# Optimization experiments

Hardware: AMD Instinct MI355X
Metric: run time of the kernel (lower is better)

Reference implementation:

```python
import jax, jax.numpy as jnp
import numpy as np


def setup_inputs() -> dict:
    key = jax.random.key(0)
    k1, k2, k3, k4 = jax.random.split(key, 4)
    B, S, D = 32, 512, 768
    return {
        "image": jax.random.normal(k1, (B, S, D), dtype=jnp.float32),
        "text": jax.random.normal(k2, (B, S, D), dtype=jnp.float32),
        "target": jax.random.normal(k3, (B, S, D), dtype=jnp.float32),
        "padding_mask": jax.random.randint(k4, (B, S), 0, 2, dtype=jnp.int32),
    }


def reference(image, text, target, padding_mask):
    D = image.shape[-1]
    # Drop BOS / CLS position for the text<->target alignment.
    txt = text[:, 1:]                      # [B, S-1, D]
    tgt = target[:, 1:]                    # [B, S-1, D]
    pm = padding_mask[:, 1:]               # [B, S-1]

    # Cosine similarity: normalize then batched matmul.
    txt_n = txt / jnp.linalg.norm(txt, axis=-1, keepdims=True)
    tgt_n = tgt / jnp.linalg.norm(tgt, axis=-1, keepdims=True)
    sim = jnp.einsum('bid,bjd->bij', txt_n, tgt_n)   # [B, S-1, S-1]

    # For each text token, pick the best-matching target patch.
    idx = jnp.argmax(sim, axis=-1)                   # [B, S-1]
    aligned = jnp.take_along_axis(tgt, idx[..., None], axis=1)  # [B, S-1, D]

    # Masked MSE over non-padded tokens (mask==1 means padded in torch code).
    valid = (pm == 0).astype(jnp.float32)            # [B, S-1]
    diff2 = jnp.square(txt.astype(jnp.float32) - aligned.astype(jnp.float32))
    kd_text_loss = jnp.sum(diff2 * valid[..., None]) / (jnp.sum(valid) * D)

    # Plain MSE between image tokens and full target.
    kd_image_loss = jnp.mean(jnp.square(image.astype(jnp.float32) - target.astype(jnp.float32)))

    total_loss = (kd_text_loss + kd_image_loss) / 2
    return total_loss, kd_text_loss, kd_image_loss, idx
```

## Files before the change

kernel.cpp:

```cpp
#include <hip/hip_runtime.h>
#include <math.h>

#define B       32
#define S_FULL  512
#define S       511
#define D       768
#define NROWS   (B * S)

#define TM 128
#define TN 128
#define NCHUNK 4
#define NKT 24
#define EPS_MARGIN 6e-5f
#define SIM_SCALE  512.0f
#define SIM_SCALE2 (SIM_SCALE * SIM_SCALE)

#define NPREP   (B * S_FULL / 4)
#define NRBLK   512

typedef __attribute__((ext_vector_type(8))) _Float16 f16x8;
typedef __attribute__((ext_vector_type(4))) float f32x4;

__device__ inline void cvt8(const float4& v0, const float4& v1, float s,
                            f16x8& hv, f16x8& lv) {
    float x[8] = {v0.x, v0.y, v0.z, v0.w, v1.x, v1.y, v1.z, v1.w};
    #pragma unroll
    for (int e = 0; e < 8; ++e) {
        float xs = x[e] * s;
        _Float16 h = (_Float16)xs;
        hv[e] = h;
        lv[e] = (_Float16)(xs - (float)h);
    }
}

__global__ __launch_bounds__(256) void prep_kernel(
    const float* __restrict__ image, const float* __restrict__ text,
    const float* __restrict__ target,
    float* __restrict__ inv_t, float* __restrict__ inv_g, float* __restrict__ pimg,
    float* __restrict__ ctrl)
{
    __shared__ float warr[4];
    if (blockIdx.x == 0) ctrl[threadIdx.x] = 0.f;
    int w    = threadIdx.x >> 6;
    int row  = blockIdx.x * 4 + w;
    int lane = threadIdx.x & 63;
    int b = row >> 9, i = row & 511;
    const float4* pi4 = (const float4*)(image  + (size_t)row * D);
    const float4* pt4 = (const float4*)(text   + (size_t)row * D);
    const float4* pg4 = (const float4*)(target + (size_t)row * D);
    float st = 0.f, sg = 0.f, si = 0.f;
    #pragma unroll
    for (int q = 0; q < 3; ++q) {
        float4 a = pt4[lane + 64 * q];
        float4 g = pg4[lane + 64 * q];
        float4 m = pi4[lane + 64 * q];
        st += a.x*a.x + a.y*a.y + a.z*a.z + a.w*a.w;
        sg += g.x*g.x + g.y*g.y + g.z*g.z + g.w*g.w;
        float dx = m.x-g.x, dy = m.y-g.y, dz = m.z-g.z, dw = m.w-g.w;
        si += dx*dx + dy*dy + dz*dz + dw*dw;
    }
    #pragma unroll
    for (int m = 32; m > 0; m >>= 1) {
        st += __shfl_xor(st, m); sg += __shfl_xor(sg, m); si += __shfl_xor(si, m);
    }
    if (lane == 0) {
        warr[w] = si;
        if (i >= 1) {
            int r = b * S + i - 1;
            inv_t[r] = (st > 0.f) ? 1.f / sqrtf(st) : 0.f;
            inv_g[r] = (sg > 0.f) ? 1.f / sqrtf(sg) : 0.f;
        }
    }
    __syncthreads();
    if (threadIdx.x == 0)
        pimg[blockIdx.x] = warr[0] + warr[1] + warr[2] + warr[3];
}

__global__ __launch_bounds__(256, 2) void simargmax_kernel(
    const float* __restrict__ text, const float* __restrict__ target,
    const float* __restrict__ inv_t, const float* __restrict__ inv_g,
    float* __restrict__ pv, float* __restrict__ ps, int* __restrict__ pj)
{
    __shared__ __align__(16) _Float16 As[TM * 64];
    __shared__ __align__(16) _Float16 Bs[TM * 64];

    const int i0 = blockIdx.x * TM;
    const int jc = blockIdx.y;
    const int j0 = jc * TN;
    const int b  = blockIdx.z;
    const int t  = threadIdx.x;
    const int lane = t & 63;
    const int wy = t >> 6;
    const int quad = lane >> 4, cid = lane & 15;

    const float* Abase = text   + (size_t)b * S_FULL * D + D;
    const float* Bbase = target + (size_t)b * S_FULL * D + D;

    const int r0 = t >> 2;
    const int c0 = t & 3;
    const int kq = c0 * 8;

    float sa[2], sb[2];
    #pragma unroll
    for (int h = 0; h < 2; ++h) {
        int gi = i0 + r0 + 64 * h;
        sa[h] = (gi < S) ? inv_t[b * S + gi] * SIM_SCALE : 0.f;
        int gj = j0 + r0 + 64 * h;
        sb[h] = (gj < S) ? inv_g[b * S + gj] * SIM_SCALE : 0.f;
    }

    const int sw8 = (r0 & 7) * 8;
    const int fw8 = (cid & 7) * 8;
    const int qh  = quad * 8;

    f32x4 acc[2][8];
    #pragma unroll
    for (int mt = 0; mt < 2; ++mt)
        #pragma unroll
        for (int nt = 0; nt < 8; ++nt)
            acc[mt][nt] = (f32x4){0.f, 0.f, 0.f, 0.f};

    for (int kt = 0; kt < NKT; ++kt) {
        const int k0 = kt * 32;
        float4 va[2][2], vb[2][2];
        #pragma unroll
        for (int h = 0; h < 2; ++h) {
            int gi = i0 + r0 + 64 * h;
            if (gi < S) {
                const float4* pa = (const float4*)(Abase + (size_t)gi * D + k0 + kq);
                va[h][0] = pa[0]; va[h][1] = pa[1];
            } else {
                va[h][0] = make_float4(0.f,0.f,0.f,0.f);
                va[h][1] = make_float4(0.f,0.f,0.f,0.f);
            }
            int gj = j0 + r0 + 64 * h;
            if (gj < S) {
                const float4* pb = (const float4*)(Bbase + (size_t)gj * D + k0 + kq);
                vb[h][0] = pb[0]; vb[h][1] = pb[1];
            } else {
                vb[h][0] = make_float4(0.f,0.f,0.f,0.f);
                vb[h][1] = make_float4(0.f,0.f,0.f,0.f);
            }
        }
        __syncthreads();
        #pragma unroll
        for (int h = 0; h < 2; ++h) {
            int base = (r0 + 64 * h) * 64;
            f16x8 hv, lv;
            cvt8(va[h][0], va[h][1], sa[h], hv, lv);
            *(f16x8*)&As[base + ((c0 * 8)      ^ sw8)] = hv;
            *(f16x8*)&As[base + ((32 + c0 * 8) ^ sw8)] = lv;
            cvt8(vb[h][0], vb[h][1], sb[h], hv, lv);
            *(f16x8*)&Bs[base + ((c0 * 8)      ^ sw8)] = hv;
            *(f16x8*)&Bs[base + ((32 + c0 * 8) ^ sw8)] = lv;
        }
        __syncthreads();

        f16x8 ah[2], al[2];
        #pragma unroll
        for (int mt = 0; mt < 2; ++mt) {
            int ad = (wy * 32 + mt * 16 + cid) * 64;
            ah[mt] = *(const f16x8*)&As[ad + ( qh       ^ fw8)];
            al[mt] = *(const f16x8*)&As[ad + ((32 + qh) ^ fw8)];
        }
        #pragma unroll
        for (int nt = 0; nt < 8; ++nt) {
            int bd = (nt * 16 + cid) * 64;
            f16x8 bh = *(const f16x8*)&Bs[bd + ( qh       ^ fw8)];
            f16x8 bl = *(const f16x8*)&Bs[bd + ((32 + qh) ^ fw8)];
            #pragma unroll
            for (int mt = 0; mt < 2; ++mt) {
                acc[mt][nt] = __builtin_amdgcn_mfma_f32_16x16x32_f16(ah[mt], bh, acc[mt][nt], 0, 0, 0);
                acc[mt][nt] = __builtin_amdgcn_mfma_f32_16x16x32_f16(ah[mt], bl, acc[mt][nt], 0, 0, 0);
                acc[mt][nt] = __builtin_amdgcn_mfma_f32_16x16x32_f16(al[mt], bh, acc[mt][nt], 0, 0, 0);
            }
        }
    }

    #pragma unroll
    for (int mt = 0; mt < 2; ++mt) {
        #pragma unroll
        for (int r = 0; r < 4; ++r) {
            float v1 = -INFINITY, v2 = -INFINITY; int j1 = -1;
            #pragma unroll
            for (int nt = 0; nt < 8; ++nt) {
                int col = j0 + nt * 16 + cid;
                float v = acc[mt][nt][r];
                if (col < S) {
                    if (v > v1) { v2 = v1; v1 = v; j1 = col; }
                    else if (v > v2) v2 = v;
                }
            }
            #pragma unroll
            for (int m = 1; m < 16; m <<= 1) {
                float ov1 = __shfl_xor(v1, m);
                int   oj1 = __shfl_xor(j1, m);
                float ov2 = __shfl_xor(v2, m);
                if (ov1 > v1) { v2 = fmaxf(v1, ov2); v1 = ov1; j1 = oj1; }
                else          { v2 = fmaxf(v2, ov1); }
            }
            if (cid == 0) {
                int gi = i0 + wy * 32 + mt * 16 + quad * 4 + r;
                if (gi < S) {
                    size_t o = ((size_t)(b * S + gi) << 2) + jc;
                    pv[o] = v1; ps[o] = v2; pj[o] = j1;
                }
            }
        }
    }
}

__global__ __launch_bounds__(256) void text_kernel(
    const float* __restrict__ text, const float* __restrict__ target,
    const int* __restrict__ pm,
    const float* __restrict__ pv, const float* __restrict__ ps, const int* __restrict__ pj,
    float* __restrict__ idx_f, float* __restrict__ acc,
    int* __restrict__ list, int* __restrict__ cnt)
{
    __shared__ float ls[4], lc[4];
    int w   = threadIdx.x >> 6;
    int row = blockIdx.x * 4 + w;
    int lane = threadIdx.x & 63;
    int b = row / S, i = row - b * S;

    float v1 = -INFINITY, v2 = -INFINITY; int j1 = 0;
    #pragma unroll
    for (int c = 0; c < NCHUNK; ++c) {
        size_t o = ((size_t)row << 2) + c;
        float a1 = pv[o], a2 = ps[o]; int aj = pj[o];
        if (a1 > v1) { v2 = fmaxf(v1, a2); v1 = a1; j1 = aj; }
        else         { v2 = fmaxf(v2, a1); }
    }

    float s = 0.f, c1 = 0.f;
    if (v1 - v2 < EPS_MARGIN * SIM_SCALE2) {
        if (lane == 0) { int p = atomicAdd(cnt, 1); list[p] = row; }
    } else {
        if (lane == 0) idx_f[row] = (float)j1;
        if (pm[b * S_FULL + i + 1] == 0) {
            const float4* pt = (const float4*)(text   + (size_t)(b * S_FULL + i  + 1) * D);
            const float4* pg = (const float4*)(target + (size_t)(b * S_FULL + j1 + 1) * D);
            #pragma unroll
            for (int q = 0; q < 3; ++q) {
                float4 a = pt[lane + 64 * q];
                float4 g = pg[lane + 64 * q];
                float dx = a.x-g.x, dy = a.y-g.y, dz = a.z-g.z, dw = a.w-g.w;
                s += dx*dx + dy*dy + dz*dz + dw*dw;
            }
            #pragma unroll
            for (int m = 32; m > 0; m >>= 1) s += __shfl_xor(s, m);
            c1 = 1.f;
        }
    }
    if (lane == 0) { ls[w] = s; lc[w] = c1; }
    __syncthreads();
    if (threadIdx.x == 0) {
        float S4 = ls[0] + ls[1] + ls[2] + ls[3];
        float C4 = lc[0] + lc[1] + lc[2] + lc[3];
        if (C4 > 0.f) {
            atomicAdd(&acc[64  + (blockIdx.x & 63)], S4);
            atomicAdd(&acc[128 + (blockIdx.x & 63)], C4);
        }
    }
}

__global__ __launch_bounds__(256) void recheck_kernel(
    const float* __restrict__ text, const float* __restrict__ target,
    const int* __restrict__ pm, const float* __restrict__ inv_g,
    const int* __restrict__ list, const int* __restrict__ cnt,
    float* __restrict__ idx_f, float* __restrict__ acc,
    int* __restrict__ done, const float* __restrict__ pimg,
    float* __restrict__ out)
{
    __shared__ float wv[4];
    __shared__ int   wj[4];
    __shared__ int   bjf;
    __shared__ int   islast;
    const int t = threadIdx.x, w = t >> 6, lane = t & 63;
    const int n = *cnt;
    for (int it = blockIdx.x; it < n; it += gridDim.x) {
        int row = list[it];
        int b = row / S, i = row - b * S;
        const float4* tp = (const float4*)(text + (size_t)(b * S_FULL + i + 1) * D);
        float4 tr0 = tp[lane], tr1 = tp[lane + 64], tr2 = tp[lane + 128];
        const float* Gb = target + (size_t)b * S_FULL * D + D;
        const float* ig = inv_g + b * S;

        float bv = -INFINITY; int bj = 0;
        for (int j = w; j < S; j += 8) {
            const float4* g0 = (const float4*)(Gb + (size_t)j * D);
            int j2 = j + 4; bool ok2 = (j2 < S);
            const float4* g1 = (const float4*)(Gb + (size_t)(ok2 ? j2 : j) * D);
            float4 a0 = g0[lane], a1 = g0[lane + 64], a2 = g0[lane + 128];
            float4 c0 = g1[lane], c1 = g1[lane + 64], c2 = g1[lane + 128];
            float s0 = tr0.x*a0.x + tr0.y*a0.y + tr0.z*a0.z + tr0.w*a0.w
                     + tr1.x*a1.x + tr1.y*a1.y + tr1.z*a1.z + tr1.w*a1.w
                     + tr2.x*a2.x + tr2.y*a2.y + tr2.z*a2.z + tr2.w*a2.w;
            float s1 = tr0.x*c0.x + tr0.y*c0.y + tr0.z*c0.z + tr0.w*c0.w
                     + tr1.x*c1.x + tr1.y*c1.y + tr1.z*c1.z + tr1.w*c1.w
                     + tr2.x*c2.x + tr2.y*c2.y + tr2.z*c2.z + tr2.w*c2.w;
            #pragma unroll
            for (int m = 32; m > 0; m >>= 1) {
                s0 += __shfl_xor(s0, m);
                s1 += __shfl_xor(s1, m);
            }
            s0 *= ig[j];
            if (s0 > bv) { bv = s0; bj = j; }
            if (ok2) {
                s1 *= ig[j2];
                if (s1 > bv) { bv = s1; bj = j2; }
            }
        }
        if (lane == 0) { wv[w] = bv; wj[w] = bj; }
        __syncthreads();
        if (t == 0) {
            float fv = wv[0]; int fj = wj[0];
            #pragma unroll
            for (int q = 1; q < 4; ++q)
                if (wv[q] > fv || (wv[q] == fv && wj[q] < fj)) { fv = wv[q]; fj = wj[q]; }
            bjf = fj;
            idx_f[row] = (float)fj;
        }
        __syncthreads();
        if (w == 0 && pm[b * S_FULL + i + 1] == 0) {
            const float4* gp = (const float4*)(Gb + (size_t)bjf * D);
            float4 a0 = gp[lane], a1 = gp[lane + 64], a2 = gp[lane + 128];
            float dx, s = 0.f;
            dx = tr0.x-a0.x; s += dx*dx;  dx = tr0.y-a0.y; s += dx*dx;
            dx = tr0.z-a0.z; s += dx*dx;  dx = tr0.w-a0.w; s += dx*dx;
            dx = tr1.x-a1.x; s += dx*dx;  dx = tr1.y-a1.y; s += dx*dx;
            dx = tr1.z-a1.z; s += dx*dx;  dx = tr1.w-a1.w; s += dx*dx;
            dx = tr2.x-a2.x; s += dx*dx;  dx = tr2.y-a2.y; s += dx*dx;
            dx = tr2.z-a2.z; s += dx*dx;  dx = tr2.w-a2.w; s += dx*dx;
            #pragma unroll
            for (int m = 32; m > 0; m >>= 1) s += __shfl_xor(s, m);
            if (lane == 0) {
                atomicAdd(&acc[64  + (blockIdx.x & 63)], s);
                atomicAdd(&acc[128 + (blockIdx.x & 63)], 1.0f);
            }
        }
        __syncthreads();
    }

    if (t == 0) {
        __threadfence();
        int prev = atomicAdd(done, 1);
        islast = (prev == (int)gridDim.x - 1);
    }
    __syncthreads();
    if (!islast) return;
    __threadfence();
    {
        __shared__ float r[12];
        float si = 0.f;
        for (int i = t; i < NPREP; i += 256) si += pimg[i];
        float st = (t < 64) ? atomicAdd(&acc[64 + t],  0.0f) : 0.f;
        float sc = (t < 64) ? atomicAdd(&acc[128 + t], 0.0f) : 0.f;
        #pragma unroll
        for (int m = 32; m > 0; m >>= 1) {
            si += __shfl_xor(si, m);
            st += __shfl_xor(st, m);
            sc += __shfl_xor(sc, m);
        }
        if (lane == 0) { r[w] = si; r[4 + w] = st; r[8 + w] = sc; }
        __syncthreads();
        if (t == 0) {
            si = r[0] + r[1] + r[2] + r[3];
            st = r[4] + r[5] + r[6] + r[7];
            sc = r[8] + r[9] + r[10] + r[11];
            float img = si / (float)((size_t)B * S_FULL * D);
            float txt = st / (sc * (float)D);
            out[0] = 0.5f * (txt + img);
            out[1] = txt;
            out[2] = img;
        }
    }
}

extern "C" void kernel_launch(void* const* d_in, const int* in_sizes, int n_in,
                              void* d_out, int out_size, void* d_ws, size_t ws_size,
                              hipStream_t stream) {
    const float* image  = (const float*)d_in[0];
    const float* text   = (const float*)d_in[1];
    const float* target = (const float*)d_in[2];
    const int*   pm     = (const int*)d_in[3];
    float* out = (float*)d_out;

    float* ws    = (float*)d_ws;
    float* inv_t = ws;
    float* inv_g = ws + NROWS;
    float* pv    = ws + 2 * NROWS;
    float* ps    = ws + 6 * NROWS;
    int*   pj    = (int*)(ws + 10 * NROWS);
    int*   list  = (int*)(ws + 14 * NROWS);
    float* ctrl  = ws + 15 * NROWS;
    int*   cnt   = (int*)ctrl;
    int*   done  = (int*)ctrl + 1;
    float* acc   = ctrl + 64;
    float* pimg  = ctrl + 256;

    prep_kernel<<<NPREP, 256, 0, stream>>>(image, text, target, inv_t, inv_g, pimg, ctrl);
    simargmax_kernel<<<dim3(4, NCHUNK, B), 256, 0, stream>>>(
        text, target, inv_t, inv_g, pv, ps, pj);
    text_kernel<<<(NROWS + 3) / 4, 256, 0, stream>>>(
        text, target, pm, pv, ps, pj, out + 3, acc, list, cnt);
    recheck_kernel<<<NRBLK, 256, 0, stream>>>(
        text, target, pm, inv_g, list, cnt, out + 3, acc, done, pimg, out);
}
```

Measured before the change: 310.2 us.

## Assign one target row per lane in recheck, staging text row in LDS

The recheck kernel now stages the text row in shared memory and gives each lane its own target row, so each lane computes a full 768-wide dot product serially. Previously each wave split one dot product across lanes and reduced it with shuffles. This removes the per-candidate shuffle reductions and keeps them only for the final argmax. In exchange, each lane now reads a separate row of target with strided, uncoalesced loads, and the order of floating-point summation changes.

Result: no change. 305.3 us (-1.6%).

```diff
diff --git a/kernel.cpp b/kernel.cpp
--- a/kernel.cpp
+++ b/kernel.cpp
@@ -272,6 +272,7 @@
     int* __restrict__ done, const float* __restrict__ pimg,
     float* __restrict__ out)
 {
+    __shared__ __align__(16) float txt_lds[D];
     __shared__ float wv[4];
     __shared__ int   wj[4];
     __shared__ int   bjf;
@@ -281,35 +282,39 @@
     for (int it = blockIdx.x; it < n; it += gridDim.x) {
         int row = list[it];
         int b = row / S, i = row - b * S;
-        const float4* tp = (const float4*)(text + (size_t)(b * S_FULL + i + 1) * D);
-        float4 tr0 = tp[lane], tr1 = tp[lane + 64], tr2 = tp[lane + 128];
+        const float4* tp4 = (const float4*)(text + (size_t)(b * S_FULL + i + 1) * D);
+        if (t < D / 4) ((float4*)txt_lds)[t] = tp4[t];
+        __syncthreads();
         const float* Gb = target + (size_t)b * S_FULL * D + D;
         const float* ig = inv_g + b * S;
+        const float4* tl = (const float4*)txt_lds;
 
         float bv = -INFINITY; int bj = 0;
-        for (int j = w; j < S; j += 8) {
-            const float4* g0 = (const float4*)(Gb + (size_t)j * D);
-            int j2 = j + 4; bool ok2 = (j2 < S);
-            const float4* g1 = (const float4*)(Gb + (size_t)(ok2 ? j2 : j) * D);
-            float4 a0 = g0[lane], a1 = g0[lane + 64], a2 = g0[lane + 128];
-            float4 c0 = g1[lane], c1 = g1[lane + 64], c2 = g1[lane + 128];
-            float s0 = tr0.x*a0.x + tr0.y*a0.y + tr0.z*a0.z + tr0.w*a0.w
-                     + tr1.x*a1.x + tr1.y*a1.y + tr1.z*a1.z + tr1.w*a1.w
-                     + tr2.x*a2.x + tr2.y*a2.y + tr2.z*a2.z + tr2.w*a2.w;
-            float s1 = tr0.x*c0.x + tr0.y*c0.y + tr0.z*c0.z + tr0.w*c0.w
-                     + tr1.x*c1.x + tr1.y*c1.y + tr1.z*c1.z + tr1.w*c1.w
-                     + tr2.x*c2.x + tr2.y*c2.y + tr2.z*c2.z + tr2.w*c2.w;
-            #pragma unroll
-            for (int m = 32; m > 0; m >>= 1) {
-                s0 += __shfl_xor(s0, m);
-                s1 += __shfl_xor(s1, m);
-            }
-            s0 *= ig[j];
-            if (s0 > bv) { bv = s0; bj = j; }
-            if (ok2) {
-                s1 *= ig[j2];
-                if (s1 > bv) { bv = s1; bj = j2; }
-            }
+        #pragma unroll
+        for (int p = 0; p < 2; ++p) {
+            int j = w * 128 + p * 64 + lane;
+            if (j < S) {
+                const float4* gp = (const float4*)(Gb + (size_t)j * D);
+                float a0 = 0.f, a1 = 0.f, a2 = 0.f, a3 = 0.f;
+                for (int d = 0; d < D / 4; d += 4) {
+                    float4 g0 = gp[d],     t0 = tl[d];
+                    float4 g1 = gp[d + 1], t1 = tl[d + 1];
+                    float4 g2 = gp[d + 2], t2 = tl[d + 2];
+                    float4 g3 = gp[d + 3], t3 = tl[d + 3];
+                    a0 += g0.x*t0.x + g0.y*t0.y + g0.z*t0.z + g0.w*t0.w;
+                    a1 += g1.x*t1.x + g1.y*t1.y + g1.z*t1.z + g1.w*t1.w;
+                    a2 += g2.x*t2.x + g2.y*t2.y + g2.z*t2.z + g2.w*t2.w;
+                    a3 += g3.x*t3.x + g3.y*t3.y + g3.z*t3.z + g3.w*t3.w;
+                }
+                float s = ((a0 + a1) + (a2 + a3)) * ig[j];
+                if (s > bv || (s == bv && j < bj)) { bv = s; bj = j; }
+            }
+        }
+        #pragma unroll
+        for (int m = 32; m > 0; m >>= 1) {
+            float ov = __shfl_xor(bv, m);
+            int   oj = __shfl_xor(bj, m);
+            if (ov > bv || (ov == bv && oj < bj)) { bv = ov; bj = oj; }
         }
         if (lane == 0) { wv[w] = bv; wj[w] = bj; }
         __syncthreads();
@@ -323,15 +328,15 @@
         }
         __syncthreads();
         if (w == 0 && pm[b * S_FULL + i + 1] == 0) {
-            const float4* gp = (const float4*)(Gb + (size_t)bjf * D);
-            float4 a0 = gp[lane], a1 = gp[lane + 64], a2 = gp[lane + 128];
-            float dx, s = 0.f;
-            dx = tr0.x-a0.x; s += dx*dx;  dx = tr0.y-a0.y; s += dx*dx;
-            dx = tr0.z-a0.z; s += dx*dx;  dx = tr0.w-a0.w; s += dx*dx;
-            dx = tr1.x-a1.x; s += dx*dx;  dx = tr1.y-a1.y; s += dx*dx;
-            dx = tr1.z-a1.z; s += dx*dx;  dx = tr1.w-a1.w; s += dx*dx;
-            dx = tr2.x-a2.x; s += dx*dx;  dx = tr2.y-a2.y; s += dx*dx;
-            dx = tr2.z-a2.z; s += dx*dx;  dx = tr2.w-a2.w; s += dx*dx;
+            const float4* gp2 = (const float4*)(Gb + (size_t)bjf * D);
+            float s = 0.f;
+            #pragma unroll
+            for (int q = 0; q < 3; ++q) {
+                float4 a = tl[lane + 64 * q];
+                float4 g = gp2[lane + 64 * q];
+                float dx = a.x-g.x, dy = a.y-g.y, dz = a.z-g.z, dw = a.w-g.w;
+                s += dx*dx + dy*dy + dz*dz + dw*dw;
+            }
             #pragma unroll
             for (int m = 32; m > 0; m >>= 1) s += __shfl_xor(s, m);
             if (lane == 0) {
```
